# Optimization experiments

Measured on AMD Instinct MI355X. Metric: run time of the kernel, lower is better.

## Reference

```python
import jax, jax.numpy as jnp
import numpy as np

H = 16        # heads
DH = 64       # dim_head
DM = 1024     # query_dim = context_dim
INNER = H * DH


def setup_inputs() -> dict:
    key = jax.random.key(0)
    ks = jax.random.split(key, 5)
    s = 0.02
    queries = jax.random.normal(ks[0], (2, 2048, DM), dtype=jnp.float32)
    Wq = jax.random.normal(ks[1], (DM, INNER), dtype=jnp.float32) * s
    Wkv = jax.random.normal(ks[2], (DM, 2 * INNER), dtype=jnp.float32) * s
    Wo = jax.random.normal(ks[3], (INNER, DM), dtype=jnp.float32) * s
    bo = jax.random.normal(ks[4], (DM,), dtype=jnp.float32) * s
    return {"queries": queries, "Wq": Wq, "Wkv": Wkv, "Wo": Wo, "bo": bo}


def reference(queries, Wq, Wkv, Wo, bo):
    b, n, _ = queries.shape
    scale = DH ** -0.5
    q = queries @ Wq                       # [b, n, inner]
    kv = queries @ Wkv                     # self-attention: context = queries
    k, v = jnp.split(kv, 2, axis=-1)
    # b n (h d) -> b h n d
    split_heads = lambda t: t.reshape(b, n, H, DH).transpose(0, 2, 1, 3)
    q, k, v = map(split_heads, (q, k, v))
    sim = jnp.einsum('bhid,bhjd->bhij', q, k) * scale
    attn = jax.nn.softmax(sim, axis=-1)    # dropout is identity (p=0 / eval)
    out = jnp.einsum('bhij,bhjd->bhid', attn, v)
    out = out.transpose(0, 2, 1, 3).reshape(b, n, INNER)
    return out @ Wo + bo
```

## Files before the change

kernel.cpp:

```cpp
#include <hip/hip_runtime.h>
#include <math.h>
#include <stdint.h>

typedef _Float16 half8v __attribute__((ext_vector_type(8)));
typedef _Float16 half4v __attribute__((ext_vector_type(4)));
typedef _Float16 half2v __attribute__((ext_vector_type(2)));
typedef __fp16 fp16x2 __attribute__((ext_vector_type(2)));
typedef float floatx4 __attribute__((ext_vector_type(4)));

#define MFMA16(a, b, c) __builtin_amdgcn_mfma_f32_16x16x32_f16(a, b, c, 0, 0, 0)

#define QSCALE 0.18033688011112f

__device__ __forceinline__ void gld_lds16(const void* g, void* l) {
  __builtin_amdgcn_global_load_lds(
      (const __attribute__((address_space(1))) uint32_t*)(uintptr_t)g,
      (__attribute__((address_space(3))) uint32_t*)(uintptr_t)l, 16, 0, 0);
}

__device__ __forceinline__ half2v pk16(float a, float b) {
  fp16x2 t = __builtin_amdgcn_cvt_pkrtz(a, b);
  return __builtin_bit_cast(half2v, t);
}

__device__ __forceinline__ int swz(int row, int blk) {
  return row * 64 + ((blk ^ (row & 7)) << 3);
}

__device__ __forceinline__ int vswz(int row, int blk) {
  return row * 32 + ((blk ^ ((row >> 1) & 3)) << 3);
}

__device__ __forceinline__ int gswz(int row, int blk) {
  return row * 32 + ((blk ^ ((row >> 1) & 3)) << 3);
}

__global__ __launch_bounds__(256) void prep(
    const float* __restrict__ X, const float* __restrict__ Wq,
    const float* __restrict__ Wkv, const float* __restrict__ Wo,
    _Float16* __restrict__ X16, _Float16* __restrict__ WqkvT,
    _Float16* __restrict__ WoT)
{
  __shared__ alignas(16) _Float16 Tt[64 * 68];
  const int bid = blockIdx.x;
  if (bid < 2048) {
    size_t gid = (size_t)bid * 256 + threadIdx.x;
    const float4* src = (const float4*)(X) + gid * 2;
    float4 a = src[0], b = src[1];
    half8v h;
    h[0]=(_Float16)a.x; h[1]=(_Float16)a.y; h[2]=(_Float16)a.z; h[3]=(_Float16)a.w;
    h[4]=(_Float16)b.x; h[5]=(_Float16)b.y; h[6]=(_Float16)b.z; h[7]=(_Float16)b.w;
    *((half8v*)X16 + gid) = h;
    return;
  }
  int b = bid - 2048;
  const float* src; _Float16* dst; int N, tk, tn;
  if (b < 256)      { src = Wq;  dst = WqkvT;                 N = 1024; tk = b & 15;        tn = b >> 4; }
  else if (b < 768) { src = Wkv; dst = WqkvT + (size_t)1024 * 1024; N = 2048; tk = (b - 256) & 15; tn = (b - 256) >> 4; }
  else              { src = Wo;  dst = WoT;                   N = 1024; tk = (b - 768) & 15; tn = (b - 768) >> 4; }

  const int t = threadIdx.x;
  {
    int kg = t >> 4, ng = t & 15;
    const float* sp = src + (size_t)(tk * 64 + kg * 4) * N + tn * 64 + ng * 4;
    float4 r0 = *(const float4*)(sp);
    float4 r1 = *(const float4*)(sp + N);
    float4 r2 = *(const float4*)(sp + 2 * N);
    float4 r3 = *(const float4*)(sp + 3 * N);
    half4v h;
    h[0]=(_Float16)r0.x; h[1]=(_Float16)r1.x; h[2]=(_Float16)r2.x; h[3]=(_Float16)r3.x;
    *(half4v*)&Tt[(ng * 4 + 0) * 68 + kg * 4] = h;
    h[0]=(_Float16)r0.y; h[1]=(_Float16)r1.y; h[2]=(_Float16)r2.y; h[3]=(_Float16)r3.y;
    *(half4v*)&Tt[(ng * 4 + 1) * 68 + kg * 4] = h;
    h[0]=(_Float16)r0.z; h[1]=(_Float16)r1.z; h[2]=(_Float16)r2.z; h[3]=(_Float16)r3.z;
    *(half4v*)&Tt[(ng * 4 + 2) * 68 + kg * 4] = h;
    h[0]=(_Float16)r0.w; h[1]=(_Float16)r1.w; h[2]=(_Float16)r2.w; h[3]=(_Float16)r3.w;
    *(half4v*)&Tt[(ng * 4 + 3) * 68 + kg * 4] = h;
  }
  __syncthreads();
  #pragma unroll
  for (int i = 0; i < 2; i++) {
    int idx = t + i * 256;
    int nl = idx >> 3, k8 = (idx & 7) * 8;
    half8v v = *(half8v*)&Tt[nl * 68 + k8];
    *(half8v*)(dst + (size_t)(tn * 64 + nl) * 1024 + tk * 64 + k8) = v;
  }
}

__global__ __launch_bounds__(256) void qkv_gemm(
    const _Float16* __restrict__ X16, const _Float16* __restrict__ WqkvT,
    _Float16* __restrict__ q_ws, _Float16* __restrict__ k_ws,
    _Float16* __restrict__ vT_ws)
{
  constexpr int K = 1024;
  __shared__ alignas(16) _Float16 Tt[128 * 136];
  _Float16* As = Tt;
  _Float16* Bs = Tt + 4096;

  const int m0 = blockIdx.x * 128;
  const int n0 = blockIdx.y * 128;

  const int tid  = threadIdx.x;
  const int wave = tid >> 6, lane = tid & 63;
  const int qd = lane >> 4, l15 = lane & 15;
  const int wr = (wave >> 1) * 64, wc = (wave & 1) * 64;
  const int r0i = tid >> 2;
  const int cbs = (((tid & 3) ^ ((r0i >> 1) & 3))) * 8;

  floatx4 acc[4][4] = {};

  for (int k0 = 0; k0 < K; k0 += 32) {
    gld_lds16(X16 + (size_t)(m0 + r0i) * K + k0 + cbs, &As[tid * 8]);
    gld_lds16(X16 + (size_t)(m0 + 64 + r0i) * K + k0 + cbs, &As[(tid + 256) * 8]);
    gld_lds16(WqkvT + (size_t)(n0 + r0i) * K + k0 + cbs, &Bs[tid * 8]);
    gld_lds16(WqkvT + (size_t)(n0 + 64 + r0i) * K + k0 + cbs, &Bs[(tid + 256) * 8]);
    __syncthreads();
    half8v a[4], b[4];
    #pragma unroll
    for (int it = 0; it < 4; it++)
      a[it] = *(half8v*)&As[gswz(wr + it * 16 + l15, qd)];
    #pragma unroll
    for (int jt = 0; jt < 4; jt++)
      b[jt] = *(half8v*)&Bs[gswz(wc + jt * 16 + l15, qd)];
    #pragma unroll
    for (int it = 0; it < 4; it++)
      #pragma unroll
      for (int jt = 0; jt < 4; jt++)
        acc[it][jt] = MFMA16(a[it], b[jt], acc[it][jt]);
    __syncthreads();
  }

  if (n0 < 2048) {
    #pragma unroll
    for (int it = 0; it < 4; it++) {
      #pragma unroll
      for (int jt = 0; jt < 4; jt++) {
        #pragma unroll
        for (int r = 0; r < 4; r++) {
          int m = m0 + wr + it * 16 + qd * 4 + r;
          int n = n0 + wc + jt * 16 + l15;
          float val = acc[it][jt][r];
          int bb = m >> 11, nn = m & 2047;
          if (n0 < 1024) {
            int h = n >> 6, d = n & 63;
            q_ws[(((size_t)bb * 16 + h) * 2048 + nn) * 64 + d] = (_Float16)(val * QSCALE);
          } else {
            int c = n - 1024, h = c >> 6, d = c & 63;
            k_ws[(((size_t)bb * 16 + h) * 2048 + nn) * 64 + d] = (_Float16)val;
          }
        }
      }
    }
  } else {
    #pragma unroll
    for (int it = 0; it < 4; it++) {
      #pragma unroll
      for (int jt = 0; jt < 4; jt++) {
        #pragma unroll
        for (int r = 0; r < 4; r++) {
          int ml = wr + it * 16 + qd * 4 + r;
          int nl = wc + jt * 16 + l15;
          Tt[nl * 136 + ml] = (_Float16)acc[it][jt][r];
        }
      }
    }
    __syncthreads();
    int row = tid >> 1;
    int mh  = (tid & 1) * 64;
    int c   = (n0 - 2048) + row;
    int bb  = m0 >> 11;
    int nnb = (m0 & 2047) + mh;
    _Float16* dstp =
        vT_ws + (((size_t)bb * 16 + (c >> 6)) * 64 + (c & 63)) * 2048 + nnb;
    #pragma unroll
    for (int i = 0; i < 8; i++)
      *(half8v*)(dstp + i * 8) = *(half8v*)&Tt[row * 136 + mh + i * 8];
  }
}

__global__ __launch_bounds__(256, 2) void attn_kernel(
    const _Float16* __restrict__ q_ws, const _Float16* __restrict__ k_ws,
    const _Float16* __restrict__ vT_ws, _Float16* __restrict__ aout)
{
  constexpr int N = 2048;
  __shared__ alignas(16) char smem[66560];
  _Float16* Kbase = (_Float16*)smem;
  _Float16* Vbase = (_Float16*)(smem + 32768);
  _Float16* PQ    = (_Float16*)(smem + 49152);

  const int id = blockIdx.x;
  const int bh = ((id >> 8) << 3) | (id & 7);
  const int qt = (id >> 3) & 31;

  const _Float16* Qp = q_ws + (size_t)bh * N * 64;
  const _Float16* Kp = k_ws + (size_t)bh * N * 64;
  const _Float16* Vp = vT_ws + (size_t)bh * 64 * N;

  const int tid = threadIdx.x, wave = tid >> 6, lane = tid & 63;
  const int qd = lane >> 4, l15 = lane & 15;
  const int q0 = qt * 64;
  const int wkv = wave * 32;

  _Float16* Ps = PQ + wave * 2048;
  _Float16* Vs = Vbase + wave * 2048;

  const int krr = lane >> 3, kcb = (lane & 7) ^ krr;
  const int vrr = lane >> 2, vcb = (lane & 3) ^ ((lane >> 3) & 3);

  auto stage_k = [&](int il, int buf) {
    const _Float16* src = Kp + (size_t)(wkv + il * 128) * 64;
    _Float16* dst = Kbase + (wave * 2 + buf) * 2048;
    #pragma unroll
    for (int j = 0; j < 4; j++)
      gld_lds16(src + (size_t)(j * 8 + krr) * 64 + kcb * 8,
                dst + (j * 64 + lane) * 8);
  };
  auto stage_v = [&](int il) {
    const _Float16* src = Vp + wkv + il * 128;
    #pragma unroll
    for (int j = 0; j < 4; j++)
      gld_lds16(src + (size_t)(j * 16 + (vrr & 15)) * N + vcb * 8,
                Vs + (j * 64 + lane) * 8);
  };

  #pragma unroll
  for (int i = 0; i < 2; i++) {
    int idx = tid + i * 256;
    int r = idx >> 3, cb = (idx ^ r) & 7;
    gld_lds16(Qp + (size_t)(q0 + r) * 64 + cb * 8, PQ + idx * 8);
  }
  stage_k(0, 0);
  stage_v(0);
  stage_k(1, 1);

  asm volatile("s_waitcnt vmcnt(12)" ::: "memory");
  __builtin_amdgcn_s_barrier();
  __builtin_amdgcn_sched_barrier(0);

  half8v qf[4][2];
  #pragma unroll
  for (int m = 0; m < 4; m++)
    #pragma unroll
    for (int ks = 0; ks < 2; ks++)
      qf[m][ks] = *(half8v*)&PQ[swz(m * 16 + l15, ks * 4 + qd)];

  asm volatile("s_waitcnt lgkmcnt(0)" ::: "memory");
  __builtin_amdgcn_s_barrier();
  __builtin_amdgcn_sched_barrier(0);

  const half8v ones = {(_Float16)1, (_Float16)1, (_Float16)1, (_Float16)1,
                       (_Float16)1, (_Float16)1, (_Float16)1, (_Float16)1};
  floatx4 o[4][4] = {};
  floatx4 ol[4] = {};

  #pragma unroll 2
  for (int i = 0; i < 16; ++i) {
    if (i < 15) asm volatile("s_waitcnt vmcnt(8)" ::: "memory");
    else        asm volatile("s_waitcnt vmcnt(4)" ::: "memory");
    __builtin_amdgcn_sched_barrier(0);

    const _Float16* Kb = Kbase + (wave * 2 + (i & 1)) * 2048;

    floatx4 s[2][4] = {};
    #pragma unroll
    for (int ks = 0; ks < 2; ks++) {
      half8v kf0 = *(half8v*)&Kb[swz(l15, ks * 4 + qd)];
      half8v kf1 = *(half8v*)&Kb[swz(16 + l15, ks * 4 + qd)];
      __builtin_amdgcn_s_setprio(1);
      #pragma unroll
      for (int m = 0; m < 4; m++) {
        s[0][m] = MFMA16(kf0, qf[m][ks], s[0][m]);
        s[1][m] = MFMA16(kf1, qf[m][ks], s[1][m]);
      }
      __builtin_amdgcn_s_setprio(0);
    }

    #pragma unroll
    for (int m = 0; m < 4; m++)
      #pragma unroll
      for (int nt = 0; nt < 2; nt++) {
        float p0 = __builtin_amdgcn_exp2f(s[nt][m][0]);
        float p1 = __builtin_amdgcn_exp2f(s[nt][m][1]);
        float p2 = __builtin_amdgcn_exp2f(s[nt][m][2]);
        float p3 = __builtin_amdgcn_exp2f(s[nt][m][3]);
        half2v h01 = pk16(p0, p1);
        half2v h23 = pk16(p2, p3);
        half4v pk;
        pk[0] = h01[0]; pk[1] = h01[1]; pk[2] = h23[0]; pk[3] = h23[1];
        *(half4v*)&Ps[vswz(m * 16 + l15, 2 * nt + (qd >> 1)) + (qd & 1) * 4] = pk;
      }

    if (i < 15) asm volatile("s_waitcnt vmcnt(4)" ::: "memory");
    else        asm volatile("s_waitcnt vmcnt(0)" ::: "memory");
    __builtin_amdgcn_sched_barrier(0);

    half8v pf[4], vfr[4];
    #pragma unroll
    for (int m = 0; m < 4; m++)
      pf[m] = *(half8v*)&Ps[vswz(m * 16 + l15, qd)];
    #pragma unroll
    for (int dt = 0; dt < 4; dt++)
      vfr[dt] = *(half8v*)&Vs[vswz(dt * 16 + l15, qd)];

    asm volatile("s_waitcnt lgkmcnt(0)" ::: "memory");
    __builtin_amdgcn_sched_barrier(0);

    if (i <= 14) stage_v(i + 1);
    if (i <= 13) stage_k(i + 2, i & 1);
    __builtin_amdgcn_sched_barrier(0);

    __builtin_amdgcn_s_setprio(1);
    #pragma unroll
    for (int m = 0; m < 4; m++)
      ol[m] = MFMA16(pf[m], ones, ol[m]);
    #pragma unroll
    for (int m = 0; m < 4; m++)
      #pragma unroll
      for (int dt = 0; dt < 4; dt++)
        o[m][dt] = MFMA16(pf[m], vfr[dt], o[m][dt]);
    __builtin_amdgcn_s_setprio(0);
  }

  __syncthreads();
  float* sc    = (float*)smem;
  float* ls_sc = (float*)(smem + 65536);
  float* myp = sc + wave * 4096;
  #pragma unroll
  for (int m = 0; m < 4; m++)
    #pragma unroll
    for (int r = 0; r < 4; r++) {
      int row = m * 16 + qd * 4 + r;
      myp[row * 64 +  0 + l15] = o[m][0][r];
      myp[row * 64 + 16 + l15] = o[m][1][r];
      myp[row * 64 + 32 + l15] = o[m][2][r];
      myp[row * 64 + 48 + l15] = o[m][3][r];
      ls_sc[wave * 64 + row] = ol[m][r];
    }
  __syncthreads();

  const int bb = bh >> 4, hh = bh & 15;
  #pragma unroll
  for (int j = 0; j < 4; j++) {
    int row = wave * 16 + j * 4 + qd;
    floatx4 a0 = *(floatx4*)&sc[(size_t)(0 * 64 + row) * 64 + l15 * 4];
    floatx4 a1 = *(floatx4*)&sc[(size_t)(1 * 64 + row) * 64 + l15 * 4];
    floatx4 a2 = *(floatx4*)&sc[(size_t)(2 * 64 + row) * 64 + l15 * 4];
    floatx4 a3 = *(floatx4*)&sc[(size_t)(3 * 64 + row) * 64 + l15 * 4];
    floatx4 sum = (a0 + a1) + (a2 + a3);
    float ls = ls_sc[row] + ls_sc[64 + row] + ls_sc[128 + row] + ls_sc[192 + row];
    float inv = 1.0f / ls;
    half2v h01 = pk16(sum[0] * inv, sum[1] * inv);
    half2v h23 = pk16(sum[2] * inv, sum[3] * inv);
    half4v hv;
    hv[0] = h01[0]; hv[1] = h01[1]; hv[2] = h23[0]; hv[3] = h23[1];
    *(half4v*)(aout + ((size_t)(bb * 2048 + q0 + row)) * 1024 + hh * 64 + l15 * 4) = hv;
  }
}

__global__ __launch_bounds__(256) void out_gemm(
    const _Float16* __restrict__ A, const _Float16* __restrict__ WoT,
    const float* __restrict__ bo, float* __restrict__ Out)
{
  constexpr int K = 1024;
  __shared__ alignas(16) _Float16 As[64 * 32];
  __shared__ alignas(16) _Float16 Bs[128 * 32];

  const int m0 = blockIdx.x * 64;
  const int n0 = blockIdx.y * 128;
  const int tid = threadIdx.x;
  const int wave = tid >> 6, lane = tid & 63;
  const int qd = lane >> 4, l15 = lane & 15;
  const int wr = (wave >> 1) * 32, wc = (wave & 1) * 64;
  const int r0i = tid >> 2;
  const int cbs = (((tid & 3) ^ ((r0i >> 1) & 3))) * 8;

  floatx4 acc[2][4] = {};

  for (int k0 = 0; k0 < K; k0 += 32) {
    gld_lds16(A + (size_t)(m0 + r0i) * K + k0 + cbs, &As[tid * 8]);
    gld_lds16(WoT + (size_t)(n0 + r0i) * K + k0 + cbs, &Bs[tid * 8]);
    gld_lds16(WoT + (size_t)(n0 + 64 + r0i) * K + k0 + cbs, &Bs[(tid + 256) * 8]);
    __syncthreads();
    half8v a[2], b[4];
    #pragma unroll
    for (int it = 0; it < 2; it++)
      a[it] = *(half8v*)&As[gswz(wr + it * 16 + l15, qd)];
    #pragma unroll
    for (int jt = 0; jt < 4; jt++)
      b[jt] = *(half8v*)&Bs[gswz(wc + jt * 16 + l15, qd)];
    #pragma unroll
    for (int it = 0; it < 2; it++)
      #pragma unroll
      for (int jt = 0; jt < 4; jt++)
        acc[it][jt] = MFMA16(a[it], b[jt], acc[it][jt]);
    __syncthreads();
  }

  #pragma unroll
  for (int it = 0; it < 2; it++) {
    #pragma unroll
    for (int jt = 0; jt < 4; jt++) {
      int n = n0 + wc + jt * 16 + l15;
      float bias = bo[n];
      #pragma unroll
      for (int r = 0; r < 4; r++) {
        int m = m0 + wr + it * 16 + qd * 4 + r;
        Out[(size_t)m * 1024 + n] = acc[it][jt][r] + bias;
      }
    }
  }
}

extern "C" void kernel_launch(void* const* d_in, const int* in_sizes, int n_in,
                              void* d_out, int out_size, void* d_ws, size_t ws_size,
                              hipStream_t stream) {
  const float* X   = (const float*)d_in[0];
  const float* Wq  = (const float*)d_in[1];
  const float* Wkv = (const float*)d_in[2];
  const float* Wo  = (const float*)d_in[3];
  const float* bo  = (const float*)d_in[4];
  float* out = (float*)d_out;

  const size_t M4 = (size_t)4 * 1024 * 1024;
  _Float16* q_ws   = (_Float16*)d_ws;
  _Float16* k_ws   = q_ws + M4;
  _Float16* vT_ws  = k_ws + M4;
  _Float16* X16    = vT_ws + M4;
  _Float16* WqkvT  = X16 + M4;
  _Float16* WoT    = WqkvT + (size_t)3 * 1024 * 1024;
  _Float16* aout   = X16;

  prep<<<3072, 256, 0, stream>>>(X, Wq, Wkv, Wo, X16, WqkvT, WoT);
  qkv_gemm<<<dim3(32, 24), 256, 0, stream>>>(X16, WqkvT, q_ws, k_ws, vT_ws);
  attn_kernel<<<1024, 256, 0, stream>>>(q_ws, k_ws, vT_ws, aout);
  out_gemm<<<dim3(64, 8), 256, 0, stream>>>(aout, WoT, bo, out);
}
```

Measured before the change: 180.4 us.

## Shrink attention LDS to fit three blocks per CU with register-staged K prefetch

Replaces the double-buffered K tile in LDS with a single buffer, prefetching the next K tile into registers and writing it to LDS after the current tile is consumed. This cuts shared memory from about 65KB to about 49KB and raises launch bounds to 3 blocks per CU. The row-sum MFMA against a ones vector is replaced by scalar accumulation plus cross-lane shuffles, and the final cross-wave reduction runs in two passes to fit the smaller LDS. The cost is extra VGPR pressure from the register staging and the scalar adds, and the K loads are exposed with less latency hiding.

New measurement: 201.9 us. +11.9%, slower.

```diff
diff --git a/kernel.cpp b/kernel.cpp
--- a/kernel.cpp
+++ b/kernel.cpp
@@ -178,15 +178,15 @@
   }
 }
 
-__global__ __launch_bounds__(256, 2) void attn_kernel(
+__global__ __launch_bounds__(256, 3) void attn_kernel(
     const _Float16* __restrict__ q_ws, const _Float16* __restrict__ k_ws,
     const _Float16* __restrict__ vT_ws, _Float16* __restrict__ aout)
 {
   constexpr int N = 2048;
-  __shared__ alignas(16) char smem[66560];
+  __shared__ alignas(16) char smem[50176];
   _Float16* Kbase = (_Float16*)smem;
-  _Float16* Vbase = (_Float16*)(smem + 32768);
-  _Float16* PQ    = (_Float16*)(smem + 49152);
+  _Float16* Vbase = (_Float16*)(smem + 16384);
+  _Float16* PQ    = (_Float16*)(smem + 32768);
 
   const int id = blockIdx.x;
   const int bh = ((id >> 8) << 3) | (id & 7);
@@ -201,25 +201,19 @@
   const int q0 = qt * 64;
   const int wkv = wave * 32;
 
+  _Float16* Ks = Kbase + wave * 2048;
+  _Float16* Vs = Vbase + wave * 2048;
   _Float16* Ps = PQ + wave * 2048;
-  _Float16* Vs = Vbase + wave * 2048;
 
   const int krr = lane >> 3, kcb = (lane & 7) ^ krr;
   const int vrr = lane >> 2, vcb = (lane & 3) ^ ((lane >> 3) & 3);
-
-  auto stage_k = [&](int il, int buf) {
-    const _Float16* src = Kp + (size_t)(wkv + il * 128) * 64;
-    _Float16* dst = Kbase + (wave * 2 + buf) * 2048;
-    #pragma unroll
-    for (int j = 0; j < 4; j++)
-      gld_lds16(src + (size_t)(j * 8 + krr) * 64 + kcb * 8,
-                dst + (j * 64 + lane) * 8);
-  };
+  const int kwr = (krr * 64 + (kcb << 3));
+
   auto stage_v = [&](int il) {
     const _Float16* src = Vp + wkv + il * 128;
     #pragma unroll
     for (int j = 0; j < 4; j++)
-      gld_lds16(src + (size_t)(j * 16 + (vrr & 15)) * N + vcb * 8,
+      gld_lds16(src + (size_t)(j * 16 + vrr) * N + vcb * 8,
                 Vs + (j * 64 + lane) * 8);
   };
 
@@ -229,11 +223,25 @@
     int r = idx >> 3, cb = (idx ^ r) & 7;
     gld_lds16(Qp + (size_t)(q0 + r) * 64 + cb * 8, PQ + idx * 8);
   }
-  stage_k(0, 0);
+  {
+    const _Float16* src = Kp + (size_t)wkv * 64;
+    #pragma unroll
+    for (int j = 0; j < 4; j++)
+      gld_lds16(src + (size_t)(j * 8 + krr) * 64 + kcb * 8,
+                Ks + (j * 64 + lane) * 8);
+  }
   stage_v(0);
-  stage_k(1, 1);
-
-  asm volatile("s_waitcnt vmcnt(12)" ::: "memory");
+  const _Float16* Kw = Kp + (size_t)wkv * 64;
+  half8v kr0, kr1, kr2, kr3;
+  {
+    const _Float16* nb = Kw + (size_t)1 * 8192 + lane * 8;
+    kr0 = *(const half8v*)(nb);
+    kr1 = *(const half8v*)(nb + 512);
+    kr2 = *(const half8v*)(nb + 1024);
+    kr3 = *(const half8v*)(nb + 1536);
+  }
+
+  asm volatile("s_waitcnt vmcnt(8)" ::: "memory");
   __builtin_amdgcn_s_barrier();
   __builtin_amdgcn_sched_barrier(0);
 
@@ -248,24 +256,15 @@
   __builtin_amdgcn_s_barrier();
   __builtin_amdgcn_sched_barrier(0);
 
-  const half8v ones = {(_Float16)1, (_Float16)1, (_Float16)1, (_Float16)1,
-                       (_Float16)1, (_Float16)1, (_Float16)1, (_Float16)1};
   floatx4 o[4][4] = {};
-  floatx4 ol[4] = {};
-
-  #pragma unroll 2
+  float lsum[4] = {};
+
   for (int i = 0; i < 16; ++i) {
-    if (i < 15) asm volatile("s_waitcnt vmcnt(8)" ::: "memory");
-    else        asm volatile("s_waitcnt vmcnt(4)" ::: "memory");
-    __builtin_amdgcn_sched_barrier(0);
-
-    const _Float16* Kb = Kbase + (wave * 2 + (i & 1)) * 2048;
-
     floatx4 s[2][4] = {};
     #pragma unroll
     for (int ks = 0; ks < 2; ks++) {
-      half8v kf0 = *(half8v*)&Kb[swz(l15, ks * 4 + qd)];
-      half8v kf1 = *(half8v*)&Kb[swz(16 + l15, ks * 4 + qd)];
+      half8v kf0 = *(half8v*)&Ks[swz(l15, ks * 4 + qd)];
+      half8v kf1 = *(half8v*)&Ks[swz(16 + l15, ks * 4 + qd)];
       __builtin_amdgcn_s_setprio(1);
       #pragma unroll
       for (int m = 0; m < 4; m++) {
@@ -283,6 +282,7 @@
         float p1 = __builtin_amdgcn_exp2f(s[nt][m][1]);
         float p2 = __builtin_amdgcn_exp2f(s[nt][m][2]);
         float p3 = __builtin_amdgcn_exp2f(s[nt][m][3]);
+        lsum[m] += (p0 + p1) + (p2 + p3);
         half2v h01 = pk16(p0, p1);
         half2v h23 = pk16(p2, p3);
         half4v pk;
@@ -294,66 +294,97 @@
     else        asm volatile("s_waitcnt vmcnt(0)" ::: "memory");
     __builtin_amdgcn_sched_barrier(0);
 
-    half8v pf[4], vfr[4];
+    half8v pf[4], vf[4];
     #pragma unroll
     for (int m = 0; m < 4; m++)
       pf[m] = *(half8v*)&Ps[vswz(m * 16 + l15, qd)];
     #pragma unroll
     for (int dt = 0; dt < 4; dt++)
-      vfr[dt] = *(half8v*)&Vs[vswz(dt * 16 + l15, qd)];
+      vf[dt] = *(half8v*)&Vs[vswz(dt * 16 + l15, qd)];
 
     asm volatile("s_waitcnt lgkmcnt(0)" ::: "memory");
     __builtin_amdgcn_sched_barrier(0);
 
-    if (i <= 14) stage_v(i + 1);
-    if (i <= 13) stage_k(i + 2, i & 1);
+    if (i < 15) {
+      _Float16* wr = Ks + kwr;
+      *(half8v*)(wr)        = kr0;
+      *(half8v*)(wr + 512)  = kr1;
+      *(half8v*)(wr + 1024) = kr2;
+      *(half8v*)(wr + 1536) = kr3;
+    }
     __builtin_amdgcn_sched_barrier(0);
 
+    if (i < 15) stage_v(i + 1);
+    if (i < 14) {
+      const _Float16* nb = Kw + (size_t)(i + 2) * 8192 + lane * 8;
+      kr0 = *(const half8v*)(nb);
+      kr1 = *(const half8v*)(nb + 512);
+      kr2 = *(const half8v*)(nb + 1024);
+      kr3 = *(const half8v*)(nb + 1536);
+    }
+    __builtin_amdgcn_sched_barrier(0);
+
     __builtin_amdgcn_s_setprio(1);
     #pragma unroll
     for (int m = 0; m < 4; m++)
-      ol[m] = MFMA16(pf[m], ones, ol[m]);
-    #pragma unroll
-    for (int m = 0; m < 4; m++)
       #pragma unroll
       for (int dt = 0; dt < 4; dt++)
-        o[m][dt] = MFMA16(pf[m], vfr[dt], o[m][dt]);
+        o[m][dt] = MFMA16(pf[m], vf[dt], o[m][dt]);
     __builtin_amdgcn_s_setprio(0);
   }
 
+  #pragma unroll
+  for (int m = 0; m < 4; m++) {
+    lsum[m] += __shfl_xor(lsum[m], 16);
+    lsum[m] += __shfl_xor(lsum[m], 32);
+  }
+
   __syncthreads();
-  float* sc    = (float*)smem;
-  float* ls_sc = (float*)(smem + 65536);
-  float* myp = sc + wave * 4096;
+  float* sc = (float*)smem;
+  float* ls = (float*)(smem + 49152);
   #pragma unroll
   for (int m = 0; m < 4; m++)
-    #pragma unroll
-    for (int r = 0; r < 4; r++) {
-      int row = m * 16 + qd * 4 + r;
-      myp[row * 64 +  0 + l15] = o[m][0][r];
-      myp[row * 64 + 16 + l15] = o[m][1][r];
-      myp[row * 64 + 32 + l15] = o[m][2][r];
-      myp[row * 64 + 48 + l15] = o[m][3][r];
-      ls_sc[wave * 64 + row] = ol[m][r];
-    }
-  __syncthreads();
+    if (qd == 0) ls[wave * 64 + m * 16 + l15] = lsum[m];
 
   const int bb = bh >> 4, hh = bh & 15;
   #pragma unroll
-  for (int j = 0; j < 4; j++) {
-    int row = wave * 16 + j * 4 + qd;
-    floatx4 a0 = *(floatx4*)&sc[(size_t)(0 * 64 + row) * 64 + l15 * 4];
-    floatx4 a1 = *(floatx4*)&sc[(size_t)(1 * 64 + row) * 64 + l15 * 4];
-    floatx4 a2 = *(floatx4*)&sc[(size_t)(2 * 64 + row) * 64 + l15 * 4];
-    floatx4 a3 = *(floatx4*)&sc[(size_t)(3 * 64 + row) * 64 + l15 * 4];
-    floatx4 sum = (a0 + a1) + (a2 + a3);
-    float ls = ls_sc[row] + ls_sc[64 + row] + ls_sc[128 + row] + ls_sc[192 + row];
-    float inv = 1.0f / ls;
-    half2v h01 = pk16(sum[0] * inv, sum[1] * inv);
-    half2v h23 = pk16(sum[2] * inv, sum[3] * inv);
-    half4v hv;
-    hv[0] = h01[0]; hv[1] = h01[1]; hv[2] = h23[0]; hv[3] = h23[1];
-    *(half4v*)(aout + ((size_t)(bb * 2048 + q0 + row)) * 1024 + hh * 64 + l15 * 4) = hv;
+  for (int pass = 0; pass < 2; pass++) {
+    float* my = sc + wave * 2176;
+    #pragma unroll
+    for (int mm = 0; mm < 2; mm++) {
+      int m = pass * 2 + mm;
+      #pragma unroll
+      for (int dt = 0; dt < 4; dt++)
+        #pragma unroll
+        for (int r = 0; r < 4; r++)
+          my[(mm * 16 + qd * 4 + r) * 68 + dt * 16 + l15] = o[m][dt][r];
+    }
+    __syncthreads();
+    {
+      int r = tid >> 3, c0 = (tid & 7) * 8;
+      int row = pass * 32 + r;
+      float lsv = ls[row] + ls[64 + row] + ls[128 + row] + ls[192 + row];
+      float inv = 1.0f / lsv;
+      float acc8[8] = {};
+      #pragma unroll
+      for (int w = 0; w < 4; w++) {
+        const float* p = sc + w * 2176 + r * 68 + c0;
+        floatx4 a = *(const floatx4*)(p);
+        floatx4 b = *(const floatx4*)(p + 4);
+        acc8[0] += a[0]; acc8[1] += a[1]; acc8[2] += a[2]; acc8[3] += a[3];
+        acc8[4] += b[0]; acc8[5] += b[1]; acc8[6] += b[2]; acc8[7] += b[3];
+      }
+      _Float16 hv[8];
+      #pragma unroll
+      for (int j = 0; j < 4; j++) {
+        half2v h = pk16(acc8[2 * j] * inv, acc8[2 * j + 1] * inv);
+        hv[2 * j] = h[0]; hv[2 * j + 1] = h[1];
+      }
+      _Float16* dst =
+          aout + ((size_t)(bb * 2048 + q0 + row)) * 1024 + hh * 64 + c0;
+      *(half8v*)dst = *(half8v*)hv;
+    }
+    if (pass == 0) __syncthreads();
   }
 }
 
```
